# Optimization experiments

Measured on AMD Instinct MI355X. Metric: run time of the kernel, lower is better.

The kernel has to match this reference:

```python
import jax, jax.numpy as jnp
import numpy as np


def _pointnet(x, w1, b1, w2, b2, w3, b3):
    # x: [B, P, 5] -> pointwise MLP then max-pool over points -> [B, 64]
    h = jax.nn.relu(x @ w1.T + b1)
    h = jax.nn.relu(h @ w2.T + b2)
    h = h @ w3.T + b3
    return h.max(axis=1)


def _lstm_layer(x, wih, whh, bih, bhh):
    # x: [B, T, D]; PyTorch gate order i, f, g, o
    B = x.shape[0]
    H = whh.shape[1]
    def step(carry, xt):
        h, c = carry
        g = xt @ wih.T + bih + h @ whh.T + bhh
        i, f, gg, o = jnp.split(g, 4, axis=-1)
        c = jax.nn.sigmoid(f) * c + jax.nn.sigmoid(i) * jnp.tanh(gg)
        h = jax.nn.sigmoid(o) * jnp.tanh(c)
        return (h, c), h
    init = (jnp.zeros((B, H), x.dtype), jnp.zeros((B, H), x.dtype))
    (h_last, _), hs = jax.lax.scan(step, init, jnp.swapaxes(x, 0, 1))
    return jnp.swapaxes(hs, 0, 1), h_last


def _edge_conv(h, mask, wt, bt, wp, bp):
    # DGL EdgeConv: h_i' = max_{j in N(i)} theta(h_j - h_i) + phi(h_i)
    # theta is linear -> max_j (Th_j) - Th_i + b_theta + phi(h_i)
    Th = h @ wt.T                       # [V,128]
    Ph = h @ wp.T + bp                  # [V,128]
    neigh_max = jnp.max(jnp.where(mask[:, :, None], Th[None, :, :], -jnp.inf), axis=1)
    return neigh_max - Th + bt + Ph


def _edge_regr(e, w1, b1, w2, b2):
    return jax.nn.sigmoid(jax.nn.relu(e @ w1.T + b1) @ w2.T + b2)


def _affinity(h, N, M, er_w1, er_b1, er_w2, er_b2):
    # faithful to source: edges[i*M+j] = h[j] - h[i]  (j indexes first M rows, as in the code)
    E = (h[None, :M, :] - h[:N, None, :]).reshape(N * M, -1)
    return _edge_regr(E, er_w1, er_b1, er_w2, er_b2).reshape(N, M)


def setup_inputs() -> dict:
    key = jax.random.key(0)
    ks = iter(jax.random.split(key, 40))
    N, M, P, T = 256, 256, 512, 10
    lin = lambda k, o, i: (jax.random.normal(k, (o, i), jnp.float32) / np.sqrt(i)).astype(jnp.float32)
    inp = {
        'det_pts': jax.random.normal(next(ks), (N, P, 5), jnp.float32),
        'det_boxes': jax.random.normal(next(ks), (N, 9), jnp.float32),
        'track_pts': jax.random.normal(next(ks), (M, P, 5), jnp.float32),
        'track_boxes': jax.random.normal(next(ks), (M, T, 9), jnp.float32),
        'adj': jax.random.randint(next(ks), (N + M, N + M), 0, 2, jnp.int32),
        'pn_w1': lin(next(ks), 64, 5), 'pn_b1': jnp.zeros((64,), jnp.float32),
        'pn_w2': lin(next(ks), 128, 64), 'pn_b2': jnp.zeros((128,), jnp.float32),
        'pn_w3': lin(next(ks), 64, 128), 'pn_b3': jnp.zeros((64,), jnp.float32),
        'dm_w1': lin(next(ks), 32, 9), 'dm_b1': jnp.zeros((32,), jnp.float32),
        'dm_w2': lin(next(ks), 64, 32), 'dm_b2': jnp.zeros((64,), jnp.float32),
        'l0_wih': lin(next(ks), 256, 9), 'l0_whh': lin(next(ks), 256, 64),
        'l0_bih': jnp.zeros((256,), jnp.float32), 'l0_bhh': jnp.zeros((256,), jnp.float32),
        'l1_wih': lin(next(ks), 256, 64), 'l1_whh': lin(next(ks), 256, 64),
        'l1_bih': jnp.zeros((256,), jnp.float32), 'l1_bhh': jnp.zeros((256,), jnp.float32),
        'gc_wt': jnp.stack([lin(next(ks), 128, 128) for _ in range(4)]),
        'gc_bt': jnp.zeros((4, 128), jnp.float32),
        'gc_wp': jnp.stack([lin(next(ks), 128, 128) for _ in range(4)]),
        'gc_bp': jnp.zeros((4, 128), jnp.float32),
        'er_w1': lin(next(ks), 64, 128), 'er_b1': jnp.zeros((64,), jnp.float32),
        'er_w2': lin(next(ks), 1, 64), 'er_b2': jnp.zeros((1,), jnp.float32),
    }
    return inp


def reference(det_pts, det_boxes, track_pts, track_boxes, adj,
              pn_w1, pn_b1, pn_w2, pn_b2, pn_w3, pn_b3,
              dm_w1, dm_b1, dm_w2, dm_b2,
              l0_wih, l0_whh, l0_bih, l0_bhh,
              l1_wih, l1_whh, l1_bih, l1_bhh,
              gc_wt, gc_bt, gc_wp, gc_bp,
              er_w1, er_b1, er_w2, er_b2):
    N, M = det_pts.shape[0], track_pts.shape[0]
    V = N + M
    # appearance features (shared PointNet)
    det_app = _pointnet(det_pts, pn_w1, pn_b1, pn_w2, pn_b2, pn_w3, pn_b3)    # [N,64]
    trk_app = _pointnet(track_pts, pn_w1, pn_b1, pn_w2, pn_b2, pn_w3, pn_b3)  # [M,64]
    # motion features
    det_mot = jax.nn.relu(det_boxes @ dm_w1.T + dm_b1) @ dm_w2.T + dm_b2      # [N,64]
    hs0, _ = _lstm_layer(track_boxes, l0_wih, l0_whh, l0_bih, l0_bhh)
    _, trk_mot = _lstm_layer(hs0, l1_wih, l1_whh, l1_bih, l1_bhh)             # [M,64]
    h = jnp.concatenate([
        jnp.concatenate([det_app, det_mot], axis=1),
        jnp.concatenate([trk_app, trk_mot], axis=1)], axis=0)                 # [V,128]
    # neighbor-source mask: edge i->j for adj[i,j]!=0, plus self-loops
    mask = (adj.T != 0) | jnp.eye(V, dtype=bool)                              # mask[i,j]: j is source neighbor of i
    aff1 = None
    for k in range(4):
        h = jax.nn.relu(_edge_conv(h, mask, gc_wt[k], gc_bt[k], gc_wp[k], gc_bp[k]))
        if k == 0:
            aff1 = _affinity(h, N, M, er_w1, er_b1, er_w2, er_b2)
    aff_final = _affinity(h, N, M, er_w1, er_b1, er_w2, er_b2)
    return jnp.stack([aff1, aff_final])  # [2, N, M]
```

## Files before the change

### kernel.cpp

```cpp
#include <hip/hip_runtime.h>
#include <math.h>

#define NDET 256
#define NTRK 256
#define NV   512
#define PPTS 512

typedef short bf16x8 __attribute__((ext_vector_type(8)));
typedef float f32x4  __attribute__((ext_vector_type(4)));

__device__ __forceinline__ float sigf(float x) { return 1.f / (1.f + __expf(-x)); }
__device__ __forceinline__ float ftanh(float x) {
    const float xc = fmaxf(fminf(x, 15.f), -15.f);
    const float e = __expf(2.f * xc);
    return (e - 1.f) / (e + 1.f);
}

__device__ __forceinline__ short f2bf(float f) {
    unsigned u = __float_as_uint(f);
    u += 0x7fffu + ((u >> 16) & 1u);
    return (short)(u >> 16);
}
__device__ __forceinline__ unsigned pack2bf(float lo, float hi) {
    return (unsigned)(unsigned short)f2bf(lo) | ((unsigned)(unsigned short)f2bf(hi) << 16);
}
__device__ __forceinline__ bf16x8 load_frag_bf16(const float* __restrict__ src) {
    const float4 a = *(const float4*)src;
    const float4 b = *(const float4*)(src + 4);
    bf16x8 r;
    r[0] = f2bf(a.x); r[1] = f2bf(a.y); r[2] = f2bf(a.z); r[3] = f2bf(a.w);
    r[4] = f2bf(b.x); r[5] = f2bf(b.y); r[6] = f2bf(b.z); r[7] = f2bf(b.w);
    return r;
}

__global__ __launch_bounds__(256) void pointnet_kernel(
    const float* __restrict__ det_pts, const float* __restrict__ track_pts,
    const float* __restrict__ w1, const float* __restrict__ b1,
    const float* __restrict__ w2, const float* __restrict__ b2,
    const float* __restrict__ w3,
    const float* __restrict__ det_boxes,
    const float* __restrict__ dw1, const float* __restrict__ db1,
    const float* __restrict__ dw2, const float* __restrict__ db2,
    float* __restrict__ pp, float* __restrict__ hout)
{
    __shared__ __align__(16) short sH1[64][72];
    __shared__ __align__(16) short sH2[64][136];
    __shared__ __align__(16) float sX[320];
    __shared__ float sW1f[64][6];
    __shared__ float sB1[64];
    __shared__ float sbox[9];
    __shared__ float sh32[32];

    const int t  = threadIdx.x;
    const int bb = blockIdx.x >> 1;
    const int s  = blockIdx.x & 1;
    const int w  = t >> 6;
    const int ln = t & 15;
    const int kq = (t >> 4) & 3;
    const float* x = ((bb < NDET) ? (det_pts + (size_t)bb * PPTS * 5)
                                  : (track_pts + (size_t)(bb - NDET) * PPTS * 5))
                     + (size_t)s * 1280;

    for (int i = t; i < 320; i += 256) sW1f[i / 5][i % 5] = w1[i];
    if (t < 64) sB1[t] = b1[t];

    bf16x8 bf2[2][2];
#pragma unroll
    for (int nt = 0; nt < 2; ++nt)
#pragma unroll
        for (int Kt = 0; Kt < 2; ++Kt)
            bf2[nt][Kt] = load_frag_bf16(w2 + (size_t)(32 * w + 16 * nt + ln) * 64 + kq * 8 + 32 * Kt);
    bf16x8 bf3[4];
#pragma unroll
    for (int Kt = 0; Kt < 4; ++Kt)
        bf3[Kt] = load_frag_bf16(w3 + (size_t)(16 * w + ln) * 128 + kq * 8 + 32 * Kt);
    float bn[2];
#pragma unroll
    for (int nt = 0; nt < 2; ++nt) bn[nt] = b2[32 * w + 16 * nt + ln];
    __syncthreads();

    float runmax[4] = {-1e30f, -1e30f, -1e30f, -1e30f};

    const int pt = t & 63;
    for (int c = 0; c < 4; ++c) {
        for (int i = t; i < 320; i += 256) sX[i] = x[c * 320 + i];
        __syncthreads();
        {
            float xv[5];
#pragma unroll
            for (int k = 0; k < 5; ++k) xv[k] = sX[pt * 5 + k];
#pragma unroll
            for (int jj = 0; jj < 8; ++jj) {
                const int d0 = w * 16 + 2 * jj;
                float a0 = sB1[d0], a1 = sB1[d0 + 1];
#pragma unroll
                for (int k = 0; k < 5; ++k) {
                    a0 = fmaf(xv[k], sW1f[d0][k], a0);
                    a1 = fmaf(xv[k], sW1f[d0 + 1][k], a1);
                }
                *(unsigned*)&sH1[pt][d0] = pack2bf(fmaxf(a0, 0.f), fmaxf(a1, 0.f));
            }
        }
        __syncthreads();
        {
            bf16x8 af[4][2];
#pragma unroll
            for (int Mt = 0; Mt < 4; ++Mt)
#pragma unroll
                for (int Kt = 0; Kt < 2; ++Kt)
                    af[Mt][Kt] = *(const bf16x8*)&sH1[16 * Mt + ln][kq * 8 + 32 * Kt];
#pragma unroll
            for (int Mt = 0; Mt < 4; ++Mt) {
#pragma unroll
                for (int nt = 0; nt < 2; ++nt) {
                    f32x4 cacc = {0.f, 0.f, 0.f, 0.f};
                    cacc = __builtin_amdgcn_mfma_f32_16x16x32_bf16(af[Mt][0], bf2[nt][0], cacc, 0, 0, 0);
                    cacc = __builtin_amdgcn_mfma_f32_16x16x32_bf16(af[Mt][1], bf2[nt][1], cacc, 0, 0, 0);
                    const int col = 32 * w + 16 * nt + ln;
#pragma unroll
                    for (int r = 0; r < 4; ++r)
                        sH2[16 * Mt + kq * 4 + r][col] = f2bf(fmaxf(cacc[r] + bn[nt], 0.f));
                }
            }
        }
        __syncthreads();
        {
#pragma unroll
            for (int Mt = 0; Mt < 4; ++Mt) {
                f32x4 cacc = {0.f, 0.f, 0.f, 0.f};
#pragma unroll
                for (int Kt = 0; Kt < 4; ++Kt) {
                    const bf16x8 a = *(const bf16x8*)&sH2[16 * Mt + ln][kq * 8 + 32 * Kt];
                    cacc = __builtin_amdgcn_mfma_f32_16x16x32_bf16(a, bf3[Kt], cacc, 0, 0, 0);
                }
#pragma unroll
                for (int r = 0; r < 4; ++r) runmax[r] = fmaxf(runmax[r], cacc[r]);
            }
        }
        __syncthreads();
    }

    float rm = fmaxf(fmaxf(runmax[0], runmax[1]), fmaxf(runmax[2], runmax[3]));
    rm = fmaxf(rm, __shfl_xor(rm, 16));
    rm = fmaxf(rm, __shfl_xor(rm, 32));
    if ((t & 63) < 16) {
        const int n = 16 * w + ln;
        pp[(size_t)blockIdx.x * 64 + n] = rm;
    }

    if (bb < NDET && s == 0) {
        if (t < 9) sbox[t] = det_boxes[bb * 9 + t];
        __syncthreads();
        if (t < 32) {
            float a = db1[t];
#pragma unroll
            for (int k = 0; k < 9; ++k) a = fmaf(dw1[t * 9 + k], sbox[k], a);
            sh32[t] = fmaxf(a, 0.f);
        }
        __syncthreads();
        if (t < 64) {
            float a = db2[t];
#pragma unroll
            for (int k = 0; k < 32; ++k) a = fmaf(dw2[t * 32 + k], sh32[k], a);
            hout[(size_t)bb * 128 + 64 + t] = a;
        }
    }
}

__global__ __launch_bounds__(256, 1) void lstm_kernel(
    const float* __restrict__ track_boxes,
    const float* __restrict__ wih0, const float* __restrict__ whh0,
    const float* __restrict__ bih0, const float* __restrict__ bhh0,
    const float* __restrict__ wih1, const float* __restrict__ whh1,
    const float* __restrict__ bih1, const float* __restrict__ bhh1,
    float* __restrict__ hout)
{
    __shared__ float sx[90];
    __shared__ float sg[256];
    __shared__ __align__(16) float sh0[64];
    __shared__ __align__(16) float sh1[64];

    const int t = threadIdx.x;
    const int m = blockIdx.x;
    const int u = t & 63;

    if (t < 90) sx[t] = track_boxes[m * 90 + t];
    if (t < 64) { sh0[t] = 0.f; sh1[t] = 0.f; }

    float w0[9];
#pragma unroll
    for (int k = 0; k < 9; ++k) w0[k] = wih0[t * 9 + k];
    float4 wr0[16], wi1[16], wr1[16];
    {
        const float4* p0 = (const float4*)(whh0 + t * 64);
        const float4* p1 = (const float4*)(wih1 + t * 64);
        const float4* p2 = (const float4*)(whh1 + t * 64);
#pragma unroll
        for (int k = 0; k < 16; ++k) { wr0[k] = p0[k]; wi1[k] = p1[k]; wr1[k] = p2[k]; }
    }
    const float bias0 = bih0[t] + bhh0[t];
    const float bias1 = bih1[t] + bhh1[t];

    float c0 = 0.f, c1 = 0.f, h1reg = 0.f;
    __syncthreads();

    for (int s = 0; s < 10; ++s) {
        {
            float acc0 = bias0, acc1 = 0.f, acc2 = 0.f, acc3 = 0.f;
#pragma unroll
            for (int k = 0; k < 9; ++k) acc0 = fmaf(w0[k], sx[s * 9 + k], acc0);
            const float4* hv = (const float4*)sh0;
#pragma unroll
            for (int k = 0; k < 16; k += 4) {
                float4 hA = hv[k], hB = hv[k + 1], hC = hv[k + 2], hD = hv[k + 3];
                acc0 = fmaf(wr0[k].x, hA.x, acc0); acc0 = fmaf(wr0[k].y, hA.y, acc0);
                acc0 = fmaf(wr0[k].z, hA.z, acc0); acc0 = fmaf(wr0[k].w, hA.w, acc0);
                acc1 = fmaf(wr0[k+1].x, hB.x, acc1); acc1 = fmaf(wr0[k+1].y, hB.y, acc1);
                acc1 = fmaf(wr0[k+1].z, hB.z, acc1); acc1 = fmaf(wr0[k+1].w, hB.w, acc1);
                acc2 = fmaf(wr0[k+2].x, hC.x, acc2); acc2 = fmaf(wr0[k+2].y, hC.y, acc2);
                acc2 = fmaf(wr0[k+2].z, hC.z, acc2); acc2 = fmaf(wr0[k+2].w, hC.w, acc2);
                acc3 = fmaf(wr0[k+3].x, hD.x, acc3); acc3 = fmaf(wr0[k+3].y, hD.y, acc3);
                acc3 = fmaf(wr0[k+3].z, hD.z, acc3); acc3 = fmaf(wr0[k+3].w, hD.w, acc3);
            }
            sg[t] = (acc0 + acc1) + (acc2 + acc3);
        }
        __syncthreads();
        if (t < 64) {
            const float gi = sg[u], gf = sg[64 + u], gg = sg[128 + u], go = sg[192 + u];
            c0 = sigf(gf) * c0 + sigf(gi) * ftanh(gg);
            sh0[u] = sigf(go) * ftanh(c0);
        }
        __syncthreads();
        {
            float acc0 = bias1, acc1 = 0.f, acc2 = 0.f, acc3 = 0.f;
            const float4* xv = (const float4*)sh0;
            const float4* hv = (const float4*)sh1;
#pragma unroll
            for (int k = 0; k < 16; k += 4) {
                float4 xA = xv[k], xB = xv[k + 1], xC = xv[k + 2], xD = xv[k + 3];
                acc0 = fmaf(wi1[k].x, xA.x, acc0); acc0 = fmaf(wi1[k].y, xA.y, acc0);
                acc0 = fmaf(wi1[k].z, xA.z, acc0); acc0 = fmaf(wi1[k].w, xA.w, acc0);
                acc1 = fmaf(wi1[k+1].x, xB.x, acc1); acc1 = fmaf(wi1[k+1].y, xB.y, acc1);
                acc1 = fmaf(wi1[k+1].z, xB.z, acc1); acc1 = fmaf(wi1[k+1].w, xB.w, acc1);
                acc2 = fmaf(wi1[k+2].x, xC.x, acc2); acc2 = fmaf(wi1[k+2].y, xC.y, acc2);
                acc2 = fmaf(wi1[k+2].z, xC.z, acc2); acc2 = fmaf(wi1[k+2].w, xC.w, acc2);
                acc3 = fmaf(wi1[k+3].x, xD.x, acc3); acc3 = fmaf(wi1[k+3].y, xD.y, acc3);
                acc3 = fmaf(wi1[k+3].z, xD.z, acc3); acc3 = fmaf(wi1[k+3].w, xD.w, acc3);
            }
#pragma unroll
            for (int k = 0; k < 16; k += 4) {
                float4 hA = hv[k], hB = hv[k + 1], hC = hv[k + 2], hD = hv[k + 3];
                acc0 = fmaf(wr1[k].x, hA.x, acc0); acc0 = fmaf(wr1[k].y, hA.y, acc0);
                acc0 = fmaf(wr1[k].z, hA.z, acc0); acc0 = fmaf(wr1[k].w, hA.w, acc0);
                acc1 = fmaf(wr1[k+1].x, hB.x, acc1); acc1 = fmaf(wr1[k+1].y, hB.y, acc1);
                acc1 = fmaf(wr1[k+1].z, hB.z, acc1); acc1 = fmaf(wr1[k+1].w, hB.w, acc1);
                acc2 = fmaf(wr1[k+2].x, hC.x, acc2); acc2 = fmaf(wr1[k+2].y, hC.y, acc2);
                acc2 = fmaf(wr1[k+2].z, hC.z, acc2); acc2 = fmaf(wr1[k+2].w, hC.w, acc2);
                acc3 = fmaf(wr1[k+3].x, hD.x, acc3); acc3 = fmaf(wr1[k+3].y, hD.y, acc3);
                acc3 = fmaf(wr1[k+3].z, hD.z, acc3); acc3 = fmaf(wr1[k+3].w, hD.w, acc3);
            }
            sg[t] = (acc0 + acc1) + (acc2 + acc3);
        }
        __syncthreads();
        if (t < 64) {
            const float gi = sg[u], gf = sg[64 + u], gg = sg[128 + u], go = sg[192 + u];
            c1 = sigf(gf) * c1 + sigf(gi) * ftanh(gg);
            h1reg = sigf(go) * ftanh(c1);
            sh1[u] = h1reg;
        }
        __syncthreads();
    }

    if (t < 64) hout[(size_t)(NDET + m) * 128 + 64 + u] = h1reg;
}

__global__ __launch_bounds__(128) void econv_gemm_kernel(
    const float* __restrict__ pp, const float* __restrict__ b3,
    const float* __restrict__ hin, const float* __restrict__ wt,
    const float* __restrict__ wp, const float* __restrict__ bp,
    float* __restrict__ Th, float* __restrict__ Ph)
{
    __shared__ __align__(16) float srow[128];
    const int t = threadIdx.x, v = blockIdx.x;
    srow[t] = (t < 64)
        ? fmaxf(pp[(size_t)v * 128 + t], pp[(size_t)v * 128 + 64 + t]) + b3[t]
        : hin[(size_t)v * 128 + t];
    __syncthreads();
    const float4* hr = (const float4*)srow;
    const float4* wtr = (const float4*)(wt + t * 128);
    const float4* wpr = (const float4*)(wp + t * 128);
    float aT = 0.f, aP = bp[t];
#pragma unroll 8
    for (int k = 0; k < 32; ++k) {
        const float4 h = hr[k];
        const float4 a = wtr[k];
        aT = fmaf(a.x, h.x, aT); aT = fmaf(a.y, h.y, aT);
        aT = fmaf(a.z, h.z, aT); aT = fmaf(a.w, h.w, aT);
        const float4 b = wpr[k];
        aP = fmaf(b.x, h.x, aP); aP = fmaf(b.y, h.y, aP);
        aP = fmaf(b.z, h.z, aP); aP = fmaf(b.w, h.w, aP);
    }
    Th[v * 128 + t] = aT;
    Ph[v * 128 + t] = aP;
}

__global__ __launch_bounds__(256) void econv_fused_kernel(
    const int* __restrict__ adj, const float* __restrict__ Th,
    const float* __restrict__ Ph, const float* __restrict__ bt,
    const float* __restrict__ wtn, const float* __restrict__ wpn,
    const float* __restrict__ bpn,
    const float* __restrict__ erw1, float* __restrict__ uu,
    float* __restrict__ Thn, float* __restrict__ Phn)
{
    __shared__ float sneg[NV];
    __shared__ __align__(16) float4 sred[8][32];
    __shared__ __align__(16) float sh[128];

    const int t = threadIdx.x, i = blockIdx.x;
    const int l32 = t & 31, grp = t >> 5;

    for (int j = t; j < NV; j += 256)
        sneg[j] = ((adj[j * NV + i] != 0) || (j == i)) ? 0.f : -3e38f;

    float thi = 0.f, phi = 0.f, btv = 0.f;
    if (t < 128) {
        thi = Th[i * 128 + t];
        phi = Ph[i * 128 + t];
        btv = bt[t];
    }
    __syncthreads();

    float4 mx = {-3e38f, -3e38f, -3e38f, -3e38f};
    const float* __restrict__ thp = Th + 4 * l32;
#pragma unroll 4
    for (int jb = 0; jb < NV; jb += 32) {
        float4 v[4];
#pragma unroll
        for (int jj = 0; jj < 4; ++jj)
            v[jj] = *(const float4*)&thp[(size_t)(jb + 4 * grp + jj) * 128];
#pragma unroll
        for (int jj = 0; jj < 4; ++jj) {
            const float s = sneg[jb + 4 * grp + jj];
            mx.x = fmaxf(mx.x, v[jj].x + s);
            mx.y = fmaxf(mx.y, v[jj].y + s);
            mx.z = fmaxf(mx.z, v[jj].z + s);
            mx.w = fmaxf(mx.w, v[jj].w + s);
        }
    }
    sred[grp][l32] = mx;
    __syncthreads();

    if (t < 128) {
        const float* rf = (const float*)sred;
        float m = rf[t];
#pragma unroll
        for (int g = 1; g < 8; ++g) m = fmaxf(m, rf[g * 128 + t]);
        sh[t] = fmaxf(m - thi + btv + phi, 0.f);
    }
    __syncthreads();

    const float4* hr = (const float4*)sh;
    if (wtn) {
        const int d = t & 127;
        const float* wsrc = (t < 128) ? wtn : wpn;
        const float4* wr = (const float4*)(wsrc + (size_t)d * 128);
        float acc = (t < 128) ? 0.f : bpn[d];
#pragma unroll 8
        for (int k = 0; k < 32; ++k) {
            const float4 h = hr[k], wv = wr[k];
            acc = fmaf(wv.x, h.x, acc); acc = fmaf(wv.y, h.y, acc);
            acc = fmaf(wv.z, h.z, acc); acc = fmaf(wv.w, h.w, acc);
        }
        if (t < 128) Thn[i * 128 + d] = acc;
        else         Phn[i * 128 + d] = acc;
    }
    if (erw1 && i < NDET && t < 64) {
        const float4* wr = (const float4*)(erw1 + (size_t)t * 128);
        float a = 0.f;
#pragma unroll 8
        for (int k = 0; k < 32; ++k) {
            const float4 h = hr[k], wv = wr[k];
            a = fmaf(wv.x, h.x, a); a = fmaf(wv.y, h.y, a);
            a = fmaf(wv.z, h.z, a); a = fmaf(wv.w, h.w, a);
        }
        uu[i * 64 + t] = a;
    }
}

__global__ __launch_bounds__(256) void edge_kernel(
    const float* __restrict__ uu1, const float* __restrict__ uu2,
    const float* __restrict__ b1, const float* __restrict__ w2,
    const float* __restrict__ b2, float* __restrict__ out)
{
    __shared__ float sui[64], sw2[64], sb1[64];
    const int t = threadIdx.x, blk = blockIdx.x;
    const float* u = (blk < NDET) ? uu1 : uu2;
    float* o = (blk < NDET) ? out : out + NDET * NTRK;
    const int i = blk & (NDET - 1);
    if (t < 64) { sui[t] = u[i * 64 + t]; sw2[t] = w2[t]; sb1[t] = b1[t]; }
    __syncthreads();
    const float4* ur = (const float4*)(u + t * 64);
    float a = b2[0];
#pragma unroll
    for (int k = 0; k < 16; ++k) {
        const float4 uv = ur[k];
        const int k4 = k * 4;
        a = fmaf(sw2[k4 + 0], fmaxf(uv.x - sui[k4 + 0] + sb1[k4 + 0], 0.f), a);
        a = fmaf(sw2[k4 + 1], fmaxf(uv.y - sui[k4 + 1] + sb1[k4 + 1], 0.f), a);
        a = fmaf(sw2[k4 + 2], fmaxf(uv.z - sui[k4 + 2] + sb1[k4 + 2], 0.f), a);
        a = fmaf(sw2[k4 + 3], fmaxf(uv.w - sui[k4 + 3] + sb1[k4 + 3], 0.f), a);
    }
    o[i * 256 + t] = 1.f / (1.f + __expf(-a));
}

extern "C" void kernel_launch(void* const* d_in, const int* in_sizes, int n_in,
                              void* d_out, int out_size, void* d_ws, size_t ws_size,
                              hipStream_t stream)
{
    const float* det_pts     = (const float*)d_in[0];
    const float* det_boxes   = (const float*)d_in[1];
    const float* track_pts   = (const float*)d_in[2];
    const float* track_boxes = (const float*)d_in[3];
    const int*   adj         = (const int*)d_in[4];
    const float* pn_w1 = (const float*)d_in[5],  *pn_b1 = (const float*)d_in[6];
    const float* pn_w2 = (const float*)d_in[7],  *pn_b2 = (const float*)d_in[8];
    const float* pn_w3 = (const float*)d_in[9],  *pn_b3 = (const float*)d_in[10];
    const float* dm_w1 = (const float*)d_in[11], *dm_b1 = (const float*)d_in[12];
    const float* dm_w2 = (const float*)d_in[13], *dm_b2 = (const float*)d_in[14];
    const float* l0_wih = (const float*)d_in[15], *l0_whh = (const float*)d_in[16];
    const float* l0_bih = (const float*)d_in[17], *l0_bhh = (const float*)d_in[18];
    const float* l1_wih = (const float*)d_in[19], *l1_whh = (const float*)d_in[20];
    const float* l1_bih = (const float*)d_in[21], *l1_bhh = (const float*)d_in[22];
    const float* gc_wt = (const float*)d_in[23], *gc_bt = (const float*)d_in[24];
    const float* gc_wp = (const float*)d_in[25], *gc_bp = (const float*)d_in[26];
    const float* er_w1 = (const float*)d_in[27], *er_b1 = (const float*)d_in[28];
    const float* er_w2 = (const float*)d_in[29], *er_b2 = (const float*)d_in[30];
    float* out = (float*)d_out;

    float* hA  = (float*)d_ws;
    float* Th  = hA  + NV * 128;
    float* Ph  = Th  + NV * 128;
    float* Th2 = Ph  + NV * 128;
    float* Ph2 = Th2 + NV * 128;
    float* uu1 = Ph2 + NV * 128;
    float* uu2 = uu1 + NDET * 64;
    float* pp  = uu2 + NDET * 64;

    pointnet_kernel<<<2 * NV, 256, 0, stream>>>(det_pts, track_pts,
        pn_w1, pn_b1, pn_w2, pn_b2, pn_w3,
        det_boxes, dm_w1, dm_b1, dm_w2, dm_b2, pp, hA);
    lstm_kernel<<<NTRK, 256, 0, stream>>>(track_boxes,
        l0_wih, l0_whh, l0_bih, l0_bhh, l1_wih, l1_whh, l1_bih, l1_bhh, hA);

    econv_gemm_kernel<<<NV, 128, 0, stream>>>(pp, pn_b3, hA,
        gc_wt, gc_wp, gc_bp, Th, Ph);

    const size_t WSZ = 128 * 128;
    econv_fused_kernel<<<NV, 256, 0, stream>>>(adj, Th, Ph, gc_bt,
        gc_wt + WSZ, gc_wp + WSZ, gc_bp + 128, er_w1, uu1, Th2, Ph2);
    econv_fused_kernel<<<NV, 256, 0, stream>>>(adj, Th2, Ph2, gc_bt + 128,
        gc_wt + 2 * WSZ, gc_wp + 2 * WSZ, gc_bp + 256, nullptr, nullptr, Th, Ph);
    econv_fused_kernel<<<NV, 256, 0, stream>>>(adj, Th, Ph, gc_bt + 256,
        gc_wt + 3 * WSZ, gc_wp + 3 * WSZ, gc_bp + 384, nullptr, nullptr, Th2, Ph2);
    econv_fused_kernel<<<NV, 256, 0, stream>>>(adj, Th2, Ph2, gc_bt + 384,
        nullptr, nullptr, nullptr, er_w1, uu2, nullptr, nullptr);

    edge_kernel<<<NV, 256, 0, stream>>>(uu1, uu2, er_b1, er_w2, er_b2, out);
}
```

Before: 237.8 us.

## Split PointNet over four blocks per cloud and fold first affinity into econv

Result: no change. 239.7 us (+0.8%).

```diff
diff --git a/kernel.cpp b/kernel.cpp
--- a/kernel.cpp
+++ b/kernel.cpp
@@ -52,14 +52,14 @@
     __shared__ float sh32[32];
 
     const int t  = threadIdx.x;
-    const int bb = blockIdx.x >> 1;
-    const int s  = blockIdx.x & 1;
+    const int bb = blockIdx.x >> 2;
+    const int s  = blockIdx.x & 3;
     const int w  = t >> 6;
     const int ln = t & 15;
     const int kq = (t >> 4) & 3;
     const float* x = ((bb < NDET) ? (det_pts + (size_t)bb * PPTS * 5)
                                   : (track_pts + (size_t)(bb - NDET) * PPTS * 5))
-                     + (size_t)s * 1280;
+                     + (size_t)s * 640;
 
     for (int i = t; i < 320; i += 256) sW1f[i / 5][i % 5] = w1[i];
     if (t < 64) sB1[t] = b1[t];
@@ -82,7 +82,7 @@
     float runmax[4] = {-1e30f, -1e30f, -1e30f, -1e30f};
 
     const int pt = t & 63;
-    for (int c = 0; c < 4; ++c) {
+    for (int c = 0; c < 2; ++c) {
         for (int i = t; i < 320; i += 256) sX[i] = x[c * 320 + i];
         __syncthreads();
         {
@@ -282,9 +282,13 @@
 {
     __shared__ __align__(16) float srow[128];
     const int t = threadIdx.x, v = blockIdx.x;
-    srow[t] = (t < 64)
-        ? fmaxf(pp[(size_t)v * 128 + t], pp[(size_t)v * 128 + 64 + t]) + b3[t]
-        : hin[(size_t)v * 128 + t];
+    if (t < 64) {
+        const float m01 = fmaxf(pp[(size_t)v * 256 + t], pp[(size_t)v * 256 + 64 + t]);
+        const float m23 = fmaxf(pp[(size_t)v * 256 + 128 + t], pp[(size_t)v * 256 + 192 + t]);
+        srow[t] = fmaxf(m01, m23) + b3[t];
+    } else {
+        srow[t] = hin[(size_t)v * 128 + t];
+    }
     __syncthreads();
     const float4* hr = (const float4*)srow;
     const float4* wtr = (const float4*)(wt + t * 128);
@@ -310,11 +314,15 @@
     const float* __restrict__ wtn, const float* __restrict__ wpn,
     const float* __restrict__ bpn,
     const float* __restrict__ erw1, float* __restrict__ uu,
-    float* __restrict__ Thn, float* __restrict__ Phn)
+    float* __restrict__ Thn, float* __restrict__ Phn,
+    const float* __restrict__ uu_e, const float* __restrict__ eb1,
+    const float* __restrict__ ew2, const float* __restrict__ eb2,
+    float* __restrict__ aff)
 {
     __shared__ float sneg[NV];
     __shared__ __align__(16) float4 sred[8][32];
     __shared__ __align__(16) float sh[128];
+    __shared__ float sui[64], sw2[64], sb1[64];
 
     const int t = threadIdx.x, i = blockIdx.x;
     const int l32 = t & 31, grp = t >> 5;
@@ -385,18 +393,32 @@
         }
         uu[i * 64 + t] = a;
     }
+
+    if (aff && i < NDET) {
+        if (t < 64) { sui[t] = uu_e[i * 64 + t]; sw2[t] = ew2[t]; sb1[t] = eb1[t]; }
+        __syncthreads();
+        const float4* ur = (const float4*)(uu_e + (size_t)t * 64);
+        float a = eb2[0];
+#pragma unroll
+        for (int k = 0; k < 16; ++k) {
+            const float4 uv = ur[k];
+            const int k4 = k * 4;
+            a = fmaf(sw2[k4 + 0], fmaxf(uv.x - sui[k4 + 0] + sb1[k4 + 0], 0.f), a);
+            a = fmaf(sw2[k4 + 1], fmaxf(uv.y - sui[k4 + 1] + sb1[k4 + 1], 0.f), a);
+            a = fmaf(sw2[k4 + 2], fmaxf(uv.z - sui[k4 + 2] + sb1[k4 + 2], 0.f), a);
+            a = fmaf(sw2[k4 + 3], fmaxf(uv.w - sui[k4 + 3] + sb1[k4 + 3], 0.f), a);
+        }
+        aff[i * 256 + t] = 1.f / (1.f + __expf(-a));
+    }
 }
 
 __global__ __launch_bounds__(256) void edge_kernel(
-    const float* __restrict__ uu1, const float* __restrict__ uu2,
-    const float* __restrict__ b1, const float* __restrict__ w2,
-    const float* __restrict__ b2, float* __restrict__ out)
+    const float* __restrict__ u, const float* __restrict__ b1,
+    const float* __restrict__ w2, const float* __restrict__ b2,
+    float* __restrict__ out)
 {
     __shared__ float sui[64], sw2[64], sb1[64];
-    const int t = threadIdx.x, blk = blockIdx.x;
-    const float* u = (blk < NDET) ? uu1 : uu2;
-    float* o = (blk < NDET) ? out : out + NDET * NTRK;
-    const int i = blk & (NDET - 1);
+    const int t = threadIdx.x, i = blockIdx.x;
     if (t < 64) { sui[t] = u[i * 64 + t]; sw2[t] = w2[t]; sb1[t] = b1[t]; }
     __syncthreads();
     const float4* ur = (const float4*)(u + t * 64);
@@ -410,7 +432,7 @@
         a = fmaf(sw2[k4 + 2], fmaxf(uv.z - sui[k4 + 2] + sb1[k4 + 2], 0.f), a);
         a = fmaf(sw2[k4 + 3], fmaxf(uv.w - sui[k4 + 3] + sb1[k4 + 3], 0.f), a);
     }
-    o[i * 256 + t] = 1.f / (1.f + __expf(-a));
+    out[i * 256 + t] = 1.f / (1.f + __expf(-a));
 }
 
 extern "C" void kernel_launch(void* const* d_in, const int* in_sizes, int n_in,
@@ -446,7 +468,7 @@
     float* uu2 = uu1 + NDET * 64;
     float* pp  = uu2 + NDET * 64;
 
-    pointnet_kernel<<<2 * NV, 256, 0, stream>>>(det_pts, track_pts,
+    pointnet_kernel<<<4 * NV, 256, 0, stream>>>(det_pts, track_pts,
         pn_w1, pn_b1, pn_w2, pn_b2, pn_w3,
         det_boxes, dm_w1, dm_b1, dm_w2, dm_b2, pp, hA);
     lstm_kernel<<<NTRK, 256, 0, stream>>>(track_boxes,
@@ -457,13 +479,17 @@
 
     const size_t WSZ = 128 * 128;
     econv_fused_kernel<<<NV, 256, 0, stream>>>(adj, Th, Ph, gc_bt,
-        gc_wt + WSZ, gc_wp + WSZ, gc_bp + 128, er_w1, uu1, Th2, Ph2);
+        gc_wt + WSZ, gc_wp + WSZ, gc_bp + 128, er_w1, uu1, Th2, Ph2,
+        nullptr, nullptr, nullptr, nullptr, nullptr);
     econv_fused_kernel<<<NV, 256, 0, stream>>>(adj, Th2, Ph2, gc_bt + 128,
-        gc_wt + 2 * WSZ, gc_wp + 2 * WSZ, gc_bp + 256, nullptr, nullptr, Th, Ph);
+        gc_wt + 2 * WSZ, gc_wp + 2 * WSZ, gc_bp + 256, nullptr, nullptr, Th, Ph,
+        uu1, er_b1, er_w2, er_b2, out);
     econv_fused_kernel<<<NV, 256, 0, stream>>>(adj, Th, Ph, gc_bt + 256,
-        gc_wt + 3 * WSZ, gc_wp + 3 * WSZ, gc_bp + 384, nullptr, nullptr, Th2, Ph2);
-    econv_fused_kernel<<<NV, 256, 0, stream>>>(adj, Th2, Ph2, gc_bt + 384,
-        nullptr, nullptr, nullptr, er_w1, uu2, nullptr, nullptr);
-
-    edge_kernel<<<NV, 256, 0, stream>>>(uu1, uu2, er_b1, er_w2, er_b2, out);
-}
+        gc_wt + 3 * WSZ, gc_wp + 3 * WSZ, gc_bp + 384, nullptr, nullptr, Th2, Ph2,
+        nullptr, nullptr, nullptr, nullptr, nullptr);
+    econv_fused_kernel<<<NDET, 256, 0, stream>>>(adj, Th2, Ph2, gc_bt + 384,
+        nullptr, nullptr, nullptr, er_w1, uu2, nullptr, nullptr,
+        nullptr, nullptr, nullptr, nullptr, nullptr);
+
+    edge_kernel<<<NDET, 256, 0, stream>>>(uu2, er_b1, er_w2, er_b2, out + NDET * NTRK);
+}
```
